# Performance work log

Hardware: AMD Instinct MI355X
Metric: run time of the kernel (lower is better)

Reference implementation:

```python
import jax, jax.numpy as jnp
import numpy as np

N = 8192      # nodes
F = 256       # in_features
H = 64        # hidden_dim
NEG = -9e15   # mask fill value from the torch source
EPS = 1e-5    # LayerNorm eps (torch default)


def setup_inputs() -> dict:
    key = jax.random.key(0)
    ks = jax.random.split(key, 6)
    x = jax.random.normal(ks[0], (N, F), jnp.float32)
    adj = jax.random.randint(ks[1], (N, N), 0, 2, jnp.int32)
    # Linear params (xavier-ish scale, zero bias as in reset_parameters)
    Wt = jax.random.normal(ks[2], (H, F), jnp.float32) * (1.0 / np.sqrt(F))
    bt = jnp.zeros((H,), jnp.float32)
    Wa = jax.random.normal(ks[3], (1, H), jnp.float32) * (1.0 / np.sqrt(H))
    ba = jnp.zeros((1,), jnp.float32)
    Wp = jax.random.normal(ks[4], (F, H), jnp.float32) * (1.0 / np.sqrt(H))
    bp = jnp.zeros((F,), jnp.float32)
    gamma = jnp.ones((F,), jnp.float32)
    beta = jnp.zeros((F,), jnp.float32)
    return dict(x=x, adj=adj, Wt=Wt, bt=bt, Wa=Wa, ba=ba,
                Wp=Wp, bp=bp, gamma=gamma, beta=beta)


def reference(x, adj, Wt, bt, Wa, ba, Wp, bp, gamma, beta):
    # h = feature_transform(x): [N, H]
    h = x @ Wt.T + bt
    # per-source-node scalar score, expanded over all N columns: [N, 1]
    s = jax.nn.leaky_relu(h @ Wa.T + ba, negative_slope=0.2)
    # adjacency-masked softmax over neighbors (dim=1); s broadcasts to [N, N]
    scores = jnp.where(adj > 0, s, jnp.float32(NEG))
    w = jax.nn.softmax(scores, axis=1)            # [N, N]
    # dropout inactive at inference -> identity
    neighbor = w @ h                               # [N, H]
    tf = neighbor @ Wp.T + bp                      # [N, F]
    # residual + LayerNorm
    y = x + tf
    mu = jnp.mean(y, axis=-1, keepdims=True)
    var = jnp.var(y, axis=-1, keepdims=True)
    return gamma * (y - mu) * jax.lax.rsqrt(var + EPS) + beta
```

## Files before the change

kernel.cpp:

```cpp
#include <hip/hip_runtime.h>
#include <stdint.h>

#define NN 8192
#define FF 256
#define HH 64

typedef __attribute__((ext_vector_type(8))) short bf16x8;
typedef __attribute__((ext_vector_type(4))) float f32x4;

__device__ __forceinline__ uint16_t f2bf(float f) {
  union { float f; uint32_t i; } c; c.f = f;
  uint32_t r = c.i + 0x7FFFu + ((c.i >> 16) & 1u);
  return (uint16_t)(r >> 16);
}

__global__ __launch_bounds__(256) void k1_h(
    const float* __restrict__ x, const float* __restrict__ Wt,
    const float* __restrict__ bt, float* __restrict__ h,
    float* __restrict__ nb_sum, int* __restrict__ deg_g) {
  __shared__ float wtT[256 * 65];
  __shared__ float sbt[64];
  const int t = threadIdx.x;
  const int lane = t & 63;
  const int w = t >> 6;

  for (int i = 0; i < 64; ++i)
    wtT[t * 65 + i] = Wt[(size_t)i * FF + t];
  if (t < 64) sbt[t] = bt[t];
  __syncthreads();

  const int r0 = blockIdx.x * 32 + w * 8;
  const float binit = sbt[lane];
  float acc[8];
#pragma unroll
  for (int r = 0; r < 8; ++r) acc[r] = binit;

  for (int f4 = 0; f4 < FF; f4 += 4) {
    float4 xs[8];
#pragma unroll
    for (int r = 0; r < 8; ++r)
      xs[r] = *(const float4*)(x + (size_t)(r0 + r) * FF + f4);
    const float wt0 = wtT[(f4 + 0) * 65 + lane];
    const float wt1 = wtT[(f4 + 1) * 65 + lane];
    const float wt2 = wtT[(f4 + 2) * 65 + lane];
    const float wt3 = wtT[(f4 + 3) * 65 + lane];
#pragma unroll
    for (int r = 0; r < 8; ++r)
      acc[r] += xs[r].x * wt0 + xs[r].y * wt1 + xs[r].z * wt2 + xs[r].w * wt3;
  }
#pragma unroll
  for (int r = 0; r < 8; ++r)
    h[(size_t)(r0 + r) * HH + lane] = acc[r];

  float4 z = {0.f, 0.f, 0.f, 0.f};
  float4* nbz = (float4*)(nb_sum + (size_t)blockIdx.x * 32 * HH);
  for (int i = t; i < 512; i += 256) nbz[i] = z;
  if (t < 32) deg_g[blockIdx.x * 32 + t] = 0;
}

__global__ __launch_bounds__(256) void k1b_hT(
    const float* __restrict__ h, uint16_t* __restrict__ hT) {
  __shared__ float s[64][65];
  const int t = threadIdx.x;
  const int n0 = blockIdx.x * 64;
  for (int i = 0; i < 16; ++i) {
    int idx = i * 256 + t;
    int r = idx >> 6, c = idx & 63;
    s[r][c] = h[(size_t)(n0 + r) * HH + c];
  }
  __syncthreads();
  for (int i = 0; i < 16; ++i) {
    int idx = i * 256 + t;
    int c = idx >> 6, n = idx & 63;
    hT[(size_t)c * NN + n0 + n] = f2bf(s[n][c]);
  }
}

__global__ __launch_bounds__(256) void k2_attn(
    const int* __restrict__ adj, const uint16_t* __restrict__ hT,
    float* __restrict__ nb_sum, int* __restrict__ deg_g) {
  __shared__ float s_part[4][16][64];
  __shared__ int   s_deg[16];

  const int t    = threadIdx.x;
  const int w    = t >> 6;
  const int lane = t & 63;
  const int m    = lane & 15;
  const int q    = lane >> 4;
  const int g    = blockIdx.x >> 1;
  const int half = blockIdx.x & 1;
  const int row0 = g * 16;

  if (t < 16) s_deg[t] = 0;
  __syncthreads();

  const int kbeg = half * (NN / 2) + w * (NN / 8);
  const int kend = kbeg + (NN / 8);

  f32x4 acc0 = 0, acc1 = 0, acc2 = 0, acc3 = 0;
  int degm = 0;
  const int* __restrict__ arow = adj + (size_t)(row0 + m) * NN;
  const uint16_t* __restrict__ hrow = hT + (size_t)m * NN;

  for (int kb = kbeg; kb < kend; kb += 64) {
    const int k0 = kb + q * 8;
    const int k1 = k0 + 32;
    int4 a0 = *(const int4*)(arow + k0);
    int4 a1 = *(const int4*)(arow + k0 + 4);
    int4 a2 = *(const int4*)(arow + k1);
    int4 a3 = *(const int4*)(arow + k1 + 4);
    bf16x8 b0 = *(const bf16x8*)(hrow + k0);
    bf16x8 b1 = *(const bf16x8*)(hrow + 16 * NN + k0);
    bf16x8 b2 = *(const bf16x8*)(hrow + 32 * NN + k0);
    bf16x8 b3 = *(const bf16x8*)(hrow + 48 * NN + k0);
    bf16x8 c0 = *(const bf16x8*)(hrow + k1);
    bf16x8 c1 = *(const bf16x8*)(hrow + 16 * NN + k1);
    bf16x8 c2 = *(const bf16x8*)(hrow + 32 * NN + k1);
    bf16x8 c3 = *(const bf16x8*)(hrow + 48 * NN + k1);
    bf16x8 afA;
    afA[0] = a0.x ? (short)0x3F80 : (short)0;
    afA[1] = a0.y ? (short)0x3F80 : (short)0;
    afA[2] = a0.z ? (short)0x3F80 : (short)0;
    afA[3] = a0.w ? (short)0x3F80 : (short)0;
    afA[4] = a1.x ? (short)0x3F80 : (short)0;
    afA[5] = a1.y ? (short)0x3F80 : (short)0;
    afA[6] = a1.z ? (short)0x3F80 : (short)0;
    afA[7] = a1.w ? (short)0x3F80 : (short)0;
    bf16x8 afB;
    afB[0] = a2.x ? (short)0x3F80 : (short)0;
    afB[1] = a2.y ? (short)0x3F80 : (short)0;
    afB[2] = a2.z ? (short)0x3F80 : (short)0;
    afB[3] = a2.w ? (short)0x3F80 : (short)0;
    afB[4] = a3.x ? (short)0x3F80 : (short)0;
    afB[5] = a3.y ? (short)0x3F80 : (short)0;
    afB[6] = a3.z ? (short)0x3F80 : (short)0;
    afB[7] = a3.w ? (short)0x3F80 : (short)0;
    acc0 = __builtin_amdgcn_mfma_f32_16x16x32_bf16(afA, b0, acc0, 0, 0, 0);
    acc1 = __builtin_amdgcn_mfma_f32_16x16x32_bf16(afA, b1, acc1, 0, 0, 0);
    acc2 = __builtin_amdgcn_mfma_f32_16x16x32_bf16(afA, b2, acc2, 0, 0, 0);
    acc3 = __builtin_amdgcn_mfma_f32_16x16x32_bf16(afA, b3, acc3, 0, 0, 0);
    acc0 = __builtin_amdgcn_mfma_f32_16x16x32_bf16(afB, c0, acc0, 0, 0, 0);
    acc1 = __builtin_amdgcn_mfma_f32_16x16x32_bf16(afB, c1, acc1, 0, 0, 0);
    acc2 = __builtin_amdgcn_mfma_f32_16x16x32_bf16(afB, c2, acc2, 0, 0, 0);
    acc3 = __builtin_amdgcn_mfma_f32_16x16x32_bf16(afB, c3, acc3, 0, 0, 0);
    degm += a0.x + a0.y + a0.z + a0.w + a1.x + a1.y + a1.z + a1.w;
    degm += a2.x + a2.y + a2.z + a2.w + a3.x + a3.y + a3.z + a3.w;
  }

  degm += __shfl_down(degm, 32, 64);
  degm += __shfl_down(degm, 16, 64);
  if (lane < 16) atomicAdd(&s_deg[lane], degm);

#pragma unroll
  for (int rg = 0; rg < 4; ++rg) {
    s_part[w][q * 4 + rg][ 0 + m] = acc0[rg];
    s_part[w][q * 4 + rg][16 + m] = acc1[rg];
    s_part[w][q * 4 + rg][32 + m] = acc2[rg];
    s_part[w][q * 4 + rg][48 + m] = acc3[rg];
  }
  __syncthreads();

  for (int idx = t; idx < 16 * 64; idx += 256) {
    int r = idx >> 6, c = idx & 63;
    float s = s_part[0][r][c] + s_part[1][r][c] +
              s_part[2][r][c] + s_part[3][r][c];
    atomicAdd(&nb_sum[(size_t)(row0 + r) * HH + c], s);
  }
  if (t < 16) atomicAdd(&deg_g[row0 + t], s_deg[t]);
}

__global__ __launch_bounds__(256) void k3_epi(
    const float* __restrict__ x, const float* __restrict__ nb_sum,
    const int* __restrict__ deg_g, const float* __restrict__ Wp,
    const float* __restrict__ bp, const float* __restrict__ gamma,
    const float* __restrict__ beta, float* __restrict__ out) {
  __shared__ float s_nb[16][64];
  __shared__ float s_y[16 * 256];

  const int t    = threadIdx.x;
  const int w    = t >> 6;
  const int lane = t & 63;
  const int row0 = blockIdx.x * 16;

  for (int idx = t; idx < 16 * 64; idx += 256) {
    int r = idx >> 6, c = idx & 63;
    int d = deg_g[row0 + r];
    float s = nb_sum[(size_t)(row0 + r) * HH + c];
    s_nb[r][c] = (d > 0) ? s / (float)d : 0.f;
  }
  __syncthreads();

  {
    const int f = t;
    float wp[64];
    const float* wrow = Wp + (size_t)f * HH;
#pragma unroll
    for (int j = 0; j < 16; ++j) {
      float4 v = *(const float4*)(wrow + j * 4);
      wp[j * 4 + 0] = v.x; wp[j * 4 + 1] = v.y;
      wp[j * 4 + 2] = v.z; wp[j * 4 + 3] = v.w;
    }
    const float bpf = bp[f];
    for (int r = 0; r < 16; ++r) {
      float a = bpf;
#pragma unroll
      for (int k = 0; k < 64; k += 4) {
        float4 nv = *(const float4*)&s_nb[r][k];
        a += nv.x * wp[k] + nv.y * wp[k + 1] + nv.z * wp[k + 2] + nv.w * wp[k + 3];
      }
      float y = x[(size_t)(row0 + r) * FF + f] + a;
      s_y[r * 256 + f] = y;
    }
  }
  __syncthreads();

  for (int i = 0; i < 4; ++i) {
    const int r = w * 4 + i;
    float4 v = *(const float4*)&s_y[r * 256 + lane * 4];
    float sum = v.x + v.y + v.z + v.w;
    float ss  = v.x * v.x + v.y * v.y + v.z * v.z + v.w * v.w;
#pragma unroll
    for (int o = 32; o >= 1; o >>= 1) {
      sum += __shfl_xor(sum, o, 64);
      ss  += __shfl_xor(ss, o, 64);
    }
    const float mu  = sum * (1.0f / 256.0f);
    const float var = ss * (1.0f / 256.0f) - mu * mu;
    const float rs  = rsqrtf(var + 1e-5f);
    const int f0 = lane * 4;
    float4 g = *(const float4*)(gamma + f0);
    float4 b = *(const float4*)(beta + f0);
    float4 o4;
    o4.x = g.x * (v.x - mu) * rs + b.x;
    o4.y = g.y * (v.y - mu) * rs + b.y;
    o4.z = g.z * (v.z - mu) * rs + b.z;
    o4.w = g.w * (v.w - mu) * rs + b.w;
    *(float4*)(out + (size_t)(row0 + r) * FF + f0) = o4;
  }
}

extern "C" void kernel_launch(void* const* d_in, const int* in_sizes, int n_in,
                              void* d_out, int out_size, void* d_ws, size_t ws_size,
                              hipStream_t stream) {
  const float* x     = (const float*)d_in[0];
  const int*   adj   = (const int*)d_in[1];
  const float* Wt    = (const float*)d_in[2];
  const float* bt    = (const float*)d_in[3];
  const float* Wp    = (const float*)d_in[6];
  const float* bp    = (const float*)d_in[7];
  const float* gamma = (const float*)d_in[8];
  const float* beta  = (const float*)d_in[9];
  float* out = (float*)d_out;

  uint16_t* hT     = (uint16_t*)d_ws;
  float*    nb_sum = (float*)((char*)d_ws + (1u << 20));
  int*      deg_g  = (int*)((char*)d_ws + (3u << 20));
  float*    h      = (float*)((char*)d_ws + (3u << 20) + (1u << 18));

  k1_h  <<<256, 256, 0, stream>>>(x, Wt, bt, h, nb_sum, deg_g);
  k1b_hT<<<128, 256, 0, stream>>>(h, hT);
  k2_attn<<<1024, 256, 0, stream>>>(adj, hT, nb_sum, deg_g);
  k3_epi<<<512, 256, 0, stream>>>(x, nb_sum, deg_g, Wp, bp, gamma, beta, out);
}
```

Before: 440.7 us.

## Pack adjacency into bitmask with degrees in a separate kernel before attention

A new kernel reads the int32 adjacency matrix once. It uses wave ballots to pack each row into 64-bit masks and computes each row's degree with popcount. The attention MFMA kernel then reads the compact bitmask instead of 32-bit adjacency values and builds the bf16 operands from bits. The degree atomics and the degree zeroing are dropped. This removes the heavy int32 stream and the degree reduction from the MFMA loop, at the cost of an extra launch and a small extra bitmask write and read.

```diff
diff --git a/kernel.cpp b/kernel.cpp
--- a/kernel.cpp
+++ b/kernel.cpp
@@ -17,7 +17,7 @@
 __global__ __launch_bounds__(256) void k1_h(
     const float* __restrict__ x, const float* __restrict__ Wt,
     const float* __restrict__ bt, float* __restrict__ h,
-    float* __restrict__ nb_sum, int* __restrict__ deg_g) {
+    float* __restrict__ nb_sum) {
   __shared__ float wtT[256 * 65];
   __shared__ float sbt[64];
   const int t = threadIdx.x;
@@ -55,7 +55,6 @@
   float4 z = {0.f, 0.f, 0.f, 0.f};
   float4* nbz = (float4*)(nb_sum + (size_t)blockIdx.x * 32 * HH);
   for (int i = t; i < 512; i += 256) nbz[i] = z;
-  if (t < 32) deg_g[blockIdx.x * 32 + t] = 0;
 }
 
 __global__ __launch_bounds__(256) void k1b_hT(
@@ -76,11 +75,31 @@
   }
 }
 
+__global__ __launch_bounds__(256) void k_pack(
+    const int* __restrict__ adj, uint64_t* __restrict__ bits,
+    int* __restrict__ deg_g) {
+  const int t = threadIdx.x;
+  const int lane = t & 63;
+  const int w = t >> 6;
+  const int row = blockIdx.x * 4 + w;
+  const int* __restrict__ arow = adj + (size_t)row * NN;
+  uint64_t* __restrict__ brow = bits + (size_t)row * (NN / 64);
+  int deg = 0;
+  for (int base = 0; base < NN; base += 64) {
+    int a = arow[base + lane];
+    uint64_t b = __ballot(a != 0);
+    if (lane == 0) {
+      brow[base >> 6] = b;
+      deg += __popcll(b);
+    }
+  }
+  if (lane == 0) deg_g[row] = deg;
+}
+
 __global__ __launch_bounds__(256) void k2_attn(
-    const int* __restrict__ adj, const uint16_t* __restrict__ hT,
-    float* __restrict__ nb_sum, int* __restrict__ deg_g) {
+    const uint64_t* __restrict__ bits, const uint16_t* __restrict__ hT,
+    float* __restrict__ nb_sum) {
   __shared__ float s_part[4][16][64];
-  __shared__ int   s_deg[16];
 
   const int t    = threadIdx.x;
   const int w    = t >> 6;
@@ -91,24 +110,17 @@
   const int half = blockIdx.x & 1;
   const int row0 = g * 16;
 
-  if (t < 16) s_deg[t] = 0;
-  __syncthreads();
-
   const int kbeg = half * (NN / 2) + w * (NN / 8);
   const int kend = kbeg + (NN / 8);
 
   f32x4 acc0 = 0, acc1 = 0, acc2 = 0, acc3 = 0;
-  int degm = 0;
-  const int* __restrict__ arow = adj + (size_t)(row0 + m) * NN;
+  const uint64_t* __restrict__ brow = bits + (size_t)(row0 + m) * (NN / 64);
   const uint16_t* __restrict__ hrow = hT + (size_t)m * NN;
 
   for (int kb = kbeg; kb < kend; kb += 64) {
     const int k0 = kb + q * 8;
     const int k1 = k0 + 32;
-    int4 a0 = *(const int4*)(arow + k0);
-    int4 a1 = *(const int4*)(arow + k0 + 4);
-    int4 a2 = *(const int4*)(arow + k1);
-    int4 a3 = *(const int4*)(arow + k1 + 4);
+    uint64_t word = brow[kb >> 6];
     bf16x8 b0 = *(const bf16x8*)(hrow + k0);
     bf16x8 b1 = *(const bf16x8*)(hrow + 16 * NN + k0);
     bf16x8 b2 = *(const bf16x8*)(hrow + 32 * NN + k0);
@@ -117,24 +129,25 @@
     bf16x8 c1 = *(const bf16x8*)(hrow + 16 * NN + k1);
     bf16x8 c2 = *(const bf16x8*)(hrow + 32 * NN + k1);
     bf16x8 c3 = *(const bf16x8*)(hrow + 48 * NN + k1);
-    bf16x8 afA;
-    afA[0] = a0.x ? (short)0x3F80 : (short)0;
-    afA[1] = a0.y ? (short)0x3F80 : (short)0;
-    afA[2] = a0.z ? (short)0x3F80 : (short)0;
-    afA[3] = a0.w ? (short)0x3F80 : (short)0;
-    afA[4] = a1.x ? (short)0x3F80 : (short)0;
-    afA[5] = a1.y ? (short)0x3F80 : (short)0;
-    afA[6] = a1.z ? (short)0x3F80 : (short)0;
-    afA[7] = a1.w ? (short)0x3F80 : (short)0;
-    bf16x8 afB;
-    afB[0] = a2.x ? (short)0x3F80 : (short)0;
-    afB[1] = a2.y ? (short)0x3F80 : (short)0;
-    afB[2] = a2.z ? (short)0x3F80 : (short)0;
-    afB[3] = a2.w ? (short)0x3F80 : (short)0;
-    afB[4] = a3.x ? (short)0x3F80 : (short)0;
-    afB[5] = a3.y ? (short)0x3F80 : (short)0;
-    afB[6] = a3.z ? (short)0x3F80 : (short)0;
-    afB[7] = a3.w ? (short)0x3F80 : (short)0;
+    const uint32_t byteA = (uint32_t)(word >> (q * 8)) & 0xFFu;
+    const uint32_t byteB = (uint32_t)(word >> (q * 8 + 32)) & 0xFFu;
+    bf16x8 afA, afB;
+    afA[0] = (byteA & 0x01u) ? (short)0x3F80 : (short)0;
+    afA[1] = (byteA & 0x02u) ? (short)0x3F80 : (short)0;
+    afA[2] = (byteA & 0x04u) ? (short)0x3F80 : (short)0;
+    afA[3] = (byteA & 0x08u) ? (short)0x3F80 : (short)0;
+    afA[4] = (byteA & 0x10u) ? (short)0x3F80 : (short)0;
+    afA[5] = (byteA & 0x20u) ? (short)0x3F80 : (short)0;
+    afA[6] = (byteA & 0x40u) ? (short)0x3F80 : (short)0;
+    afA[7] = (byteA & 0x80u) ? (short)0x3F80 : (short)0;
+    afB[0] = (byteB & 0x01u) ? (short)0x3F80 : (short)0;
+    afB[1] = (byteB & 0x02u) ? (short)0x3F80 : (short)0;
+    afB[2] = (byteB & 0x04u) ? (short)0x3F80 : (short)0;
+    afB[3] = (byteB & 0x08u) ? (short)0x3F80 : (short)0;
+    afB[4] = (byteB & 0x10u) ? (short)0x3F80 : (short)0;
+    afB[5] = (byteB & 0x20u) ? (short)0x3F80 : (short)0;
+    afB[6] = (byteB & 0x40u) ? (short)0x3F80 : (short)0;
+    afB[7] = (byteB & 0x80u) ? (short)0x3F80 : (short)0;
     acc0 = __builtin_amdgcn_mfma_f32_16x16x32_bf16(afA, b0, acc0, 0, 0, 0);
     acc1 = __builtin_amdgcn_mfma_f32_16x16x32_bf16(afA, b1, acc1, 0, 0, 0);
     acc2 = __builtin_amdgcn_mfma_f32_16x16x32_bf16(afA, b2, acc2, 0, 0, 0);
@@ -143,13 +156,7 @@
     acc1 = __builtin_amdgcn_mfma_f32_16x16x32_bf16(afB, c1, acc1, 0, 0, 0);
     acc2 = __builtin_amdgcn_mfma_f32_16x16x32_bf16(afB, c2, acc2, 0, 0, 0);
     acc3 = __builtin_amdgcn_mfma_f32_16x16x32_bf16(afB, c3, acc3, 0, 0, 0);
-    degm += a0.x + a0.y + a0.z + a0.w + a1.x + a1.y + a1.z + a1.w;
-    degm += a2.x + a2.y + a2.z + a2.w + a3.x + a3.y + a3.z + a3.w;
-  }
-
-  degm += __shfl_down(degm, 32, 64);
-  degm += __shfl_down(degm, 16, 64);
-  if (lane < 16) atomicAdd(&s_deg[lane], degm);
+  }
 
 #pragma unroll
   for (int rg = 0; rg < 4; ++rg) {
@@ -166,7 +173,6 @@
               s_part[2][r][c] + s_part[3][r][c];
     atomicAdd(&nb_sum[(size_t)(row0 + r) * HH + c], s);
   }
-  if (t < 16) atomicAdd(&deg_g[row0 + t], s_deg[t]);
 }
 
 __global__ __launch_bounds__(256) void k3_epi(
@@ -256,9 +262,11 @@
   float*    nb_sum = (float*)((char*)d_ws + (1u << 20));
   int*      deg_g  = (int*)((char*)d_ws + (3u << 20));
   float*    h      = (float*)((char*)d_ws + (3u << 20) + (1u << 18));
-
-  k1_h  <<<256, 256, 0, stream>>>(x, Wt, bt, h, nb_sum, deg_g);
+  uint64_t* bits   = (uint64_t*)((char*)d_ws + (5u << 20) + (1u << 18));
+
+  k1_h  <<<256, 256, 0, stream>>>(x, Wt, bt, h, nb_sum);
   k1b_hT<<<128, 256, 0, stream>>>(h, hT);
-  k2_attn<<<1024, 256, 0, stream>>>(adj, hT, nb_sum, deg_g);
+  k_pack<<<2048, 256, 0, stream>>>(adj, bits, deg_g);
+  k2_attn<<<1024, 256, 0, stream>>>(bits, hT, nb_sum);
   k3_epi<<<512, 256, 0, stream>>>(x, nb_sum, deg_g, Wp, bp, gamma, beta, out);
 }
```

Measured after the change: 521.2 us. 18.3% more time.
